# Optimization experiments

Hardware: AMD Instinct MI355X
Metric: run time of the kernel (lower is better)

## Reference

```python
import jax, jax.numpy as jnp
import numpy as np

D = 64          # slot_size == in_features
S = 8           # num_slots
H = 128         # mlp_hidden_size
N_ITER = 3
EPS = 1e-8


def _ln(x, g, b, eps=1e-5):
    m = jnp.mean(x, axis=-1, keepdims=True)
    v = jnp.var(x, axis=-1, keepdims=True)
    return (x - m) * jax.lax.rsqrt(v + eps) * g + b


def _gru(x, h, w_ih, w_hh, b_ih, b_hh):
    # torch.nn.GRUCell semantics, gate order r, z, n
    gi = x @ w_ih.T + b_ih
    gh = h @ w_hh.T + b_hh
    i_r, i_z, i_n = jnp.split(gi, 3, axis=-1)
    h_r, h_z, h_n = jnp.split(gh, 3, axis=-1)
    r = jax.nn.sigmoid(i_r + h_r)
    z = jax.nn.sigmoid(i_z + h_z)
    n = jnp.tanh(i_n + r * h_n)
    return (1.0 - z) * n + z * h


def setup_inputs() -> dict:
    key = jax.random.key(0)
    ks = jax.random.split(key, 16)
    sc = 0.02
    inp = {
        'inputs': jax.random.normal(ks[0], (64, 16384, D), jnp.float32),
        'slots_init': jax.random.normal(ks[1], (64, S, D), jnp.float32),
        'ln_in_g': jnp.ones((D,), jnp.float32), 'ln_in_b': jnp.zeros((D,), jnp.float32),
        'ln_s_g': jnp.ones((D,), jnp.float32), 'ln_s_b': jnp.zeros((D,), jnp.float32),
        'ln_m_g': jnp.ones((D,), jnp.float32), 'ln_m_b': jnp.zeros((D,), jnp.float32),
        'Wq': jax.random.normal(ks[2], (D, D), jnp.float32) * sc,
        'Wk': jax.random.normal(ks[3], (D, D), jnp.float32) * sc,
        'Wv': jax.random.normal(ks[4], (D, D), jnp.float32) * sc,
        'w_ih': jax.random.normal(ks[5], (3 * D, D), jnp.float32) * sc,
        'w_hh': jax.random.normal(ks[6], (3 * D, D), jnp.float32) * sc,
        'b_ih': jnp.zeros((3 * D,), jnp.float32),
        'b_hh': jnp.zeros((3 * D,), jnp.float32),
        'W1': jax.random.normal(ks[7], (H, D), jnp.float32) * sc,
        'b1': jnp.zeros((H,), jnp.float32),
        'W2': jax.random.normal(ks[8], (D, H), jnp.float32) * sc,
        'b2': jnp.zeros((D,), jnp.float32),
        'slots_mu': jax.random.normal(ks[9], (1, 1, D), jnp.float32) * sc,
        'slots_log_sigma': jax.random.normal(ks[10], (1, 1, D), jnp.float32) * sc,
    }
    return inp


def reference(inputs, slots_init, ln_in_g, ln_in_b, ln_s_g, ln_s_b, ln_m_g, ln_m_b,
              Wq, Wk, Wv, w_ih, w_hh, b_ih, b_hh, W1, b1, W2, b2,
              slots_mu, slots_log_sigma):
    B, N, _ = inputs.shape
    x = _ln(inputs, ln_in_g, ln_in_b)
    k = x @ Wk.T                               # [B, N, D]
    v = x @ Wv.T                               # [B, N, D]
    slots = slots_mu + jnp.exp(slots_log_sigma) * slots_init  # [B, S, D]
    scale = D ** -0.5
    attns = None
    for it in range(N_ITER):
        slots_prev = slots
        sn = _ln(slots, ln_s_g, ln_s_b)
        q = sn @ Wq.T                          # [B, S, D]
        logits = scale * jnp.einsum('bnd,bsd->bns', k, q)  # [B, N, S]
        attn = jax.nn.softmax(logits, axis=-1)
        if it == 0:
            attns = jax.lax.stop_gradient(attn)  # clone().detach() on first iter
        else:
            attns = attns + attn
        a = attn + EPS
        a = a / jnp.sum(a, axis=1, keepdims=True)  # normalize over inputs
        updates = jnp.einsum('bns,bnd->bsd', a, v)  # [B, S, D]
        h = _gru(updates.reshape(B * S, D), slots_prev.reshape(B * S, D),
                 w_ih, w_hh, b_ih, b_hh).reshape(B, S, D)
        mlp_out = jnp.maximum(_ln(h, ln_m_g, ln_m_b) @ W1.T + b1, 0.0) @ W2.T + b2
        slots = h + mlp_out
    return slots, attns / N_ITER
```

## Files before the change

kernel.cpp:

```cpp
#include <hip/hip_runtime.h>
#include <math.h>

#define Dk 64
#define Sk 8
#define Nk 16384
#define Bk 64
#define Hk 128
#define BSD (Bk*Sk*Dk)

typedef __attribute__((ext_vector_type(8))) short   bf16x8;
typedef __attribute__((ext_vector_type(4))) float   f32x4;
typedef __attribute__((ext_vector_type(2))) unsigned int u32x2;
typedef __attribute__((ext_vector_type(4))) unsigned int u32x4;

union FragU { u32x4 u; bf16x8 s; };

__device__ __forceinline__ unsigned short f2b(float f){
  unsigned u = __float_as_uint(f);
  unsigned r = (u + 0x7FFFu + ((u>>16)&1u)) >> 16;
  return (unsigned short)r;
}
__device__ __forceinline__ unsigned pk2(float a, float b){
  return (unsigned)f2b(a) | ((unsigned)f2b(b)<<16);
}
__device__ __forceinline__ bf16x8 mkfrag(unsigned a0,unsigned a1,unsigned a2,unsigned a3){
  FragU x; x.u = (u32x4){a0,a1,a2,a3}; return x.s;
}
__device__ __forceinline__ bf16x8 mkfrag2(u32x2 a, u32x2 b){
  FragU x; x.u = (u32x4){a.x,a.y,b.x,b.y}; return x.s;
}
__device__ __forceinline__ float wsum64(float v){
  #pragma unroll
  for (int m=1;m<64;m<<=1) v += __shfl_xor(v,m,64);
  return v;
}
__device__ __forceinline__ f32x4 ntld4(const float* p){
  return __builtin_nontemporal_load((const f32x4*)p);
}

#define MFMA16(a,b,c) __builtin_amdgcn_mfma_f32_16x16x32_bf16(a,b,c,0,0,0)
#define TRRD(dst, addr)          asm volatile("ds_read_b64_tr_b16 %0, %1"              : "=v"(dst) : "v"(addr) : "memory")
#define TRRD_O(dst, addr, OFF)   asm volatile("ds_read_b64_tr_b16 %0, %1 offset:" #OFF : "=v"(dst) : "v"(addr) : "memory")

template<int MODE, int LAST>
__global__ __launch_bounds__(256,4) void iter_kernel(
    const float* __restrict__ inp, unsigned short* __restrict__ xbf,
    const float* __restrict__ ln_g, const float* __restrict__ ln_b,
    const float* __restrict__ qtb,
    float* __restrict__ attns_out,
    float* __restrict__ Upart,
    float* __restrict__ denpart)
{
  constexpr int NQ = LAST ? 3 : 1;
  __shared__ unsigned short shmem[4*2688];
  __shared__ float ured[4][512];
  __shared__ float dred[4][8];

  const int t   = threadIdx.x;
  const int wid = t>>6, l = t&63;
  const int r16 = l&15, g = l>>4;
  unsigned short* sh = &shmem[wid*2688];
  const unsigned ldsb = (unsigned)(unsigned long long)(void*)sh;

  const int blk = blockIdx.x;
  const int gw  = blk*4 + wid;
  const int b   = gw>>6;
  const int w0  = (gw&63)*8;

  bf16x8 qf0[NQ], qf1[NQ];
  #pragma unroll
  for (int it=0; it<NQ; ++it){
    const float* qp = qtb + (size_t)it*BSD + (size_t)((b<<3) + (r16&7))*Dk + g*8;
    f32x4 a0 = *(const f32x4*)(qp);    f32x4 a1 = *(const f32x4*)(qp+4);
    f32x4 c0 = *(const f32x4*)(qp+32); f32x4 c1 = *(const f32x4*)(qp+36);
    qf0[it] = mkfrag(pk2(a0.x,a0.y),pk2(a0.z,a0.w),pk2(a1.x,a1.y),pk2(a1.z,a1.w));
    qf1[it] = mkfrag(pk2(c0.x,c0.y),pk2(c0.z,c0.w),pk2(c1.x,c1.y),pk2(c1.z,c1.w));
  }

  f32x4 uacc0={0.f,0.f,0.f,0.f}, uacc1={0.f,0.f,0.f,0.f};
  f32x4 uacc2={0.f,0.f,0.f,0.f}, uacc3={0.f,0.f,0.f,0.f};
  f32x4 dacc = {0.f,0.f,0.f,0.f};

  f32x4 gv0,gv1,gv2,gv3, bv0,bv1,bv2,bv3;
  if (MODE==0){
    const float* gp  = ln_g + g*8;      const float* bp  = ln_b + g*8;
    const float* gp2 = ln_g + 32 + g*8; const float* bp2 = ln_b + 32 + g*8;
    gv0=*(const f32x4*)gp;  gv1=*(const f32x4*)(gp+4);
    gv2=*(const f32x4*)gp2; gv3=*(const f32x4*)(gp2+4);
    bv0=*(const f32x4*)bp;  bv1=*(const f32x4*)(bp+4);
    bv2=*(const f32x4*)bp2; bv3=*(const f32x4*)(bp2+4);
  }

  f32x4 nx[2][4];
  u32x4 npA[2][2];
  u32x4 npB[2][2];
  u32x4 fr[2][2];

  auto LOADW0 = [&](int w){
    const size_t base = (size_t)b*Nk + (size_t)(w0+w)*32;
    #pragma unroll
    for (int rt=0; rt<2; ++rt){
      const size_t row = base + rt*16 + r16;
      const float* s0 = inp + row*Dk + g*8;
      const float* s1 = inp + row*Dk + 32 + g*8;
      nx[rt][0]=ntld4(s0); nx[rt][1]=ntld4(s0+4);
      nx[rt][2]=ntld4(s1); nx[rt][3]=ntld4(s1+4);
    }
  };
  auto LOADW1 = [&](int w, u32x4 (*np)[2]){
    const size_t base = (size_t)b*Nk + (size_t)(w0+w)*32;
    #pragma unroll
    for (int rt=0; rt<2; ++rt){
      const size_t row = base + rt*16 + r16;
      const unsigned short* sp = xbf + row*Dk;
      np[rt][0] = *(const u32x4*)(sp + g*8);
      np[rt][1] = *(const u32x4*)(sp + 32 + g*8);
    }
  };

  auto PROCESS = [&](int w){
    const size_t base = (size_t)b*Nk + (size_t)(w0+w)*32;
    #pragma unroll
    for (int rt=0; rt<2; ++rt){
      const int rloc = rt*16 + r16;
      u32x4 q0, q1;
      if (MODE==0){
        f32x4 x0=nx[rt][0], x1=nx[rt][1], x2=nx[rt][2], x3=nx[rt][3];
        float s1 = (x0.x+x0.y+x0.z+x0.w)+(x1.x+x1.y+x1.z+x1.w)
                 + (x2.x+x2.y+x2.z+x2.w)+(x3.x+x3.y+x3.z+x3.w);
        float s2 = x0.x*x0.x+x0.y*x0.y+x0.z*x0.z+x0.w*x0.w
                 + x1.x*x1.x+x1.y*x1.y+x1.z*x1.z+x1.w*x1.w
                 + x2.x*x2.x+x2.y*x2.y+x2.z*x2.z+x2.w*x2.w
                 + x3.x*x3.x+x3.y*x3.y+x3.z*x3.z+x3.w*x3.w;
        s1 += __shfl_xor(s1,16,64); s1 += __shfl_xor(s1,32,64);
        s2 += __shfl_xor(s2,16,64); s2 += __shfl_xor(s2,32,64);
        const float mean = s1*(1.f/64.f);
        const float rstd = rsqrtf(s2*(1.f/64.f) - mean*mean + 1e-5f);
        x0 = (x0-mean)*rstd*gv0 + bv0;  x1 = (x1-mean)*rstd*gv1 + bv1;
        x2 = (x2-mean)*rstd*gv2 + bv2;  x3 = (x3-mean)*rstd*gv3 + bv3;
        q0 = (u32x4){pk2(x0.x,x0.y),pk2(x0.z,x0.w),pk2(x1.x,x1.y),pk2(x1.z,x1.w)};
        q1 = (u32x4){pk2(x2.x,x2.y),pk2(x2.z,x2.w),pk2(x3.x,x3.y),pk2(x3.z,x3.w)};
        const size_t row = base + rloc;
        *(u32x4*)(xbf + row*Dk + g*8)      = q0;
        *(u32x4*)(xbf + row*Dk + 32 + g*8) = q1;
      } else {
        q0 = npA[rt][0]; q1 = npA[rt][1];
      }
      fr[rt][0] = q0; fr[rt][1] = q1;
      const int i0 = (g>>1)*528     + rloc*16 + (g&1)*8;
      const int i1 = ((g>>1)+2)*528 + rloc*16 + (g&1)*8;
      *(u32x4*)&sh[i0] = q0;
      *(u32x4*)&sh[i1] = q1;
    }
  };

  if (MODE==0){ LOADW0(0); PROCESS(0); LOADW0(1); }
  else if (!LAST){ LOADW1(0,npA); PROCESS(0); LOADW1(1,npA); LOADW1(2,npB); }
  else { LOADW1(0,npA); PROCESS(0); LOADW1(1,npA); }

  for (int w4=0; w4<8; ++w4){
    const size_t rowwin = (size_t)b*Nk + (size_t)(w0+w4)*32;

    #pragma unroll
    for (int rt=0; rt<2; ++rt){
      FragU fl, fh; fl.u = fr[rt][0]; fh.u = fr[rt][1];
      const bf16x8 xl = fl.s, xh = fh.s;
      f32x4 asum = {0.f,0.f,0.f,0.f};
      f32x4 atc;
      #pragma unroll
      for (int it=0; it<NQ; ++it){
        f32x4 c = {0.f,0.f,0.f,0.f};
        c = MFMA16(qf0[it], xl, c);
        c = MFMA16(qf1[it], xh, c);
        float mx = fmaxf(fmaxf(c.x,c.y), fmaxf(c.z,c.w));
        mx = fmaxf(mx, __shfl_xor(mx,16,64));
        f32x4 e;
        e.x = __expf(c.x-mx); e.y = __expf(c.y-mx);
        e.z = __expf(c.z-mx); e.w = __expf(c.w-mx);
        float es = e.x+e.y+e.z+e.w;
        es += __shfl_xor(es,16,64);
        f32x4 at = e*(1.f/es);
        if (LAST) asum = asum + at;
        atc = at;
      }
      if (LAST && l < 32){
        f32x4 nv = asum*(1.f/3.f);
        __builtin_nontemporal_store(nv,
            (f32x4*)(attns_out + (rowwin + rt*16 + r16)*Sk + g*4));
      }
      f32x4 a = atc + 1e-8f;
      dacc = dacc + a;
      u32x2 pk = {pk2(a.x,a.y), pk2(a.z,a.w)};
      *(u32x2*)&sh[2112 + (rt*16+r16)*16 + g*4] = pk;
    }

    u32x2 p0,p1, b00,b01,b10,b11,b20,b21,b30,b31;
    const unsigned xA = ldsb + g*256 + r16*2;
    const unsigned pA = ldsb + 4224 + g*256 + r16*2;
    TRRD  (b00, xA);          TRRD_O(b01, xA, 128);
    TRRD_O(b10, xA, 1056);    TRRD_O(b11, xA, 1184);
    TRRD_O(b20, xA, 2112);    TRRD_O(b21, xA, 2240);
    TRRD_O(b30, xA, 3168);    TRRD_O(b31, xA, 3296);
    TRRD  (p0, pA);           TRRD_O(p1, pA, 128);

    if (w4 < 7) PROCESS(w4+1);
    if (MODE==0){
      if (w4 < 6) LOADW0(w4+2);
    } else if (!LAST){
      if (w4 < 6){
        #pragma unroll
        for (int rt=0; rt<2; ++rt){ npA[rt][0]=npB[rt][0]; npA[rt][1]=npB[rt][1]; }
      }
      if (w4 < 5) LOADW1(w4+3, npB);
    } else {
      if (w4 < 6) LOADW1(w4+2, npA);
    }

    if (w4 < 7) asm volatile("s_waitcnt lgkmcnt(4)" ::: "memory");
    else        asm volatile("s_waitcnt lgkmcnt(0)" ::: "memory");
    __builtin_amdgcn_sched_barrier(0);

    const bf16x8 pf = mkfrag2(p0,p1);
    uacc0 = MFMA16(pf, mkfrag2(b00,b01), uacc0);
    uacc1 = MFMA16(pf, mkfrag2(b10,b11), uacc1);
    uacc2 = MFMA16(pf, mkfrag2(b20,b21), uacc2);
    uacc3 = MFMA16(pf, mkfrag2(b30,b31), uacc3);
  }

  float dd0=dacc.x, dd1=dacc.y, dd2=dacc.z, dd3=dacc.w;
  #pragma unroll
  for (int m=1;m<16;m<<=1){
    dd0 += __shfl_xor(dd0,m,64); dd1 += __shfl_xor(dd1,m,64);
    dd2 += __shfl_xor(dd2,m,64); dd3 += __shfl_xor(dd3,m,64);
  }
  if (l < 32){
    #pragma unroll
    for (int j=0;j<4;++j){
      ured[wid][(g*4+j)*64 +  0 + r16] = uacc0[j];
      ured[wid][(g*4+j)*64 + 16 + r16] = uacc1[j];
      ured[wid][(g*4+j)*64 + 32 + r16] = uacc2[j];
      ured[wid][(g*4+j)*64 + 48 + r16] = uacc3[j];
    }
    if (r16 == 0){
      dred[wid][g*4+0]=dd0; dred[wid][g*4+1]=dd1;
      dred[wid][g*4+2]=dd2; dred[wid][g*4+3]=dd3;
    }
  }
  __syncthreads();
  #pragma unroll
  for (int e=t; e<512; e+=256){
    Upart[(size_t)blk*512 + e] = ured[0][e]+ured[1][e]+ured[2][e]+ured[3][e];
  }
  if (t < 8) denpart[blk*8 + t] = dred[0][t]+dred[1][t]+dred[2][t]+dred[3][t];
}

__global__ __launch_bounds__(64) void slot_kernel(
    const float* __restrict__ slots_init,
    const float* __restrict__ mu, const float* __restrict__ lsig,
    const float* __restrict__ ln_s_g, const float* __restrict__ ln_s_b,
    const float* __restrict__ ln_m_g, const float* __restrict__ ln_m_b,
    const float* __restrict__ Wq, const float* __restrict__ Wk, const float* __restrict__ Wv,
    const float* __restrict__ w_ih, const float* __restrict__ w_hh,
    const float* __restrict__ b_ih, const float* __restrict__ b_hh,
    const float* __restrict__ W1, const float* __restrict__ b1,
    const float* __restrict__ W2, const float* __restrict__ b2,
    float* __restrict__ slots, const float* __restrict__ Upart,
    const float* __restrict__ denpart,
    float* __restrict__ qt_out, float* __restrict__ slots_out, int mode)
{
  __shared__ float sh[Hk];
  __shared__ float shh[Dk];
  const int d  = threadIdx.x;
  const int bs = blockIdx.x;

  float snew;
  if (mode == 0) {
    snew = mu[d] + expf(lsig[d]) * slots_init[bs*Dk + d];
  } else {
    const int b8 = bs>>3, s = bs&7;
    const float* up = Upart + (size_t)(b8*16)*512 + s*64 + d;
    float uval = 0.f;
    #pragma unroll
    for (int k2=0;k2<16;++k2) uval += up[(size_t)k2*512];
    float dp = (d<16) ? denpart[(b8*16 + d)*Sk + s] : 0.f;
    const float dn = wsum64(dp);

    sh[d] = uval;
    __syncthreads();
    float num = 0.f;
    #pragma unroll
    for (int j=0;j<Dk;j+=4){
      float4 w = *(const float4*)&Wv[d*Dk+j];
      num += sh[j]*w.x + sh[j+1]*w.y + sh[j+2]*w.z + sh[j+3]*w.w;
    }
    const float upd = num / dn;
    const float h = slots[bs*Dk + d];
    __syncthreads();
    sh[d] = upd; shh[d] = h;
    __syncthreads();

    float gi_r=b_ih[d], gi_z=b_ih[Dk+d], gi_n=b_ih[2*Dk+d];
    float gh_r=b_hh[d], gh_z=b_hh[Dk+d], gh_n=b_hh[2*Dk+d];
    #pragma unroll 4
    for (int j=0;j<Dk;j+=4){
      const float x0=sh[j],  x1=sh[j+1],  x2=sh[j+2],  x3=sh[j+3];
      const float h0=shh[j], h1=shh[j+1], h2=shh[j+2], h3=shh[j+3];
      float4 w;
      w = *(const float4*)&w_ih[d*Dk+j];        gi_r += x0*w.x+x1*w.y+x2*w.z+x3*w.w;
      w = *(const float4*)&w_ih[(Dk+d)*Dk+j];   gi_z += x0*w.x+x1*w.y+x2*w.z+x3*w.w;
      w = *(const float4*)&w_ih[(2*Dk+d)*Dk+j]; gi_n += x0*w.x+x1*w.y+x2*w.z+x3*w.w;
      w = *(const float4*)&w_hh[d*Dk+j];        gh_r += h0*w.x+h1*w.y+h2*w.z+h3*w.w;
      w = *(const float4*)&w_hh[(Dk+d)*Dk+j];   gh_z += h0*w.x+h1*w.y+h2*w.z+h3*w.w;
      w = *(const float4*)&w_hh[(2*Dk+d)*Dk+j]; gh_n += h0*w.x+h1*w.y+h2*w.z+h3*w.w;
    }
    const float rg = 1.f/(1.f+expf(-(gi_r+gh_r)));
    const float zg = 1.f/(1.f+expf(-(gi_z+gh_z)));
    const float ng = tanhf(gi_n + rg*gh_n);
    const float hn = (1.f-zg)*ng + zg*h;

    const float m  = wsum64(hn)*(1.f/64.f);
    const float dv = hn - m;
    const float vr = wsum64(dv*dv)*(1.f/64.f);
    const float mv = dv*rsqrtf(vr+1e-5f)*ln_m_g[d] + ln_m_b[d];
    __syncthreads();
    sh[d] = mv;
    __syncthreads();

    float h1a = b1[d], h2a = b1[Dk+d];
    #pragma unroll 4
    for (int j=0;j<Dk;j+=4){
      const float x0=sh[j], x1=sh[j+1], x2=sh[j+2], x3=sh[j+3];
      float4 w;
      w = *(const float4*)&W1[d*Dk+j];      h1a += x0*w.x+x1*w.y+x2*w.z+x3*w.w;
      w = *(const float4*)&W1[(Dk+d)*Dk+j]; h2a += x0*w.x+x1*w.y+x2*w.z+x3*w.w;
    }
    h1a = fmaxf(h1a, 0.f); h2a = fmaxf(h2a, 0.f);
    __syncthreads();
    sh[d] = h1a; sh[Dk+d] = h2a;
    __syncthreads();
    float o = b2[d];
    #pragma unroll 4
    for (int tt=0;tt<Hk;tt+=4){
      float4 w = *(const float4*)&W2[d*Hk+tt];
      o += sh[tt]*w.x + sh[tt+1]*w.y + sh[tt+2]*w.z + sh[tt+3]*w.w;
    }
    snew = hn + o;
  }

  if (slots_out){ slots_out[bs*Dk + d] = snew; return; }
  slots[bs*Dk + d] = snew;

  const float m2  = wsum64(snew)*(1.f/64.f);
  const float dv2 = snew - m2;
  const float vr2 = wsum64(dv2*dv2)*(1.f/64.f);
  const float sn  = dv2*rsqrtf(vr2+1e-5f)*ln_s_g[d] + ln_s_b[d];
  __syncthreads();
  sh[d] = sn;
  __syncthreads();
  float q = 0.f;
  #pragma unroll
  for (int j=0;j<Dk;j+=4){
    float4 w = *(const float4*)&Wq[d*Dk+j];
    q += sh[j]*w.x + sh[j+1]*w.y + sh[j+2]*w.z + sh[j+3]*w.w;
  }
  __syncthreads();
  sh[d] = q;
  __syncthreads();
  float qt = 0.f;
  for (int dd=0; dd<Dk; ++dd) qt += sh[dd]*Wk[dd*Dk + d];
  qt_out[bs*Dk + d] = qt * 0.125f;
}

extern "C" void kernel_launch(void* const* d_in, const int* in_sizes, int n_in,
                              void* d_out, int out_size, void* d_ws, size_t ws_size,
                              hipStream_t stream)
{
  const float* inp     = (const float*)d_in[0];
  const float* sinit   = (const float*)d_in[1];
  const float* ln_in_g = (const float*)d_in[2];
  const float* ln_in_b = (const float*)d_in[3];
  const float* ln_s_g  = (const float*)d_in[4];
  const float* ln_s_b  = (const float*)d_in[5];
  const float* ln_m_g  = (const float*)d_in[6];
  const float* ln_m_b  = (const float*)d_in[7];
  const float* Wq      = (const float*)d_in[8];
  const float* Wk      = (const float*)d_in[9];
  const float* Wv      = (const float*)d_in[10];
  const float* w_ih    = (const float*)d_in[11];
  const float* w_hh    = (const float*)d_in[12];
  const float* b_ih    = (const float*)d_in[13];
  const float* b_hh    = (const float*)d_in[14];
  const float* W1      = (const float*)d_in[15];
  const float* b1      = (const float*)d_in[16];
  const float* W2      = (const float*)d_in[17];
  const float* b2      = (const float*)d_in[18];
  const float* mu      = (const float*)d_in[19];
  const float* lsig    = (const float*)d_in[20];

  float* out       = (float*)d_out;
  float* out_slots = out;
  float* out_attns = out + BSD;

  char* w = (char*)d_ws;
  float* slots   = (float*)(w);
  float* qtbuf   = (float*)(w + 131072);
  float* Upart   = (float*)(w + 655360);
  float* denpart = (float*)(w + 2752512);
  unsigned short* xbf = (unsigned short*)(w + 2785280);

  float* qt0 = qtbuf;
  float* qt1 = qtbuf + BSD;
  float* qt2 = qtbuf + 2*BSD;
  float* qt3 = qtbuf + 3*BSD;

  slot_kernel<<<Bk*Sk, Dk, 0, stream>>>(sinit, mu, lsig, ln_s_g, ln_s_b, ln_m_g, ln_m_b,
      Wq, Wk, Wv, w_ih, w_hh, b_ih, b_hh, W1, b1, W2, b2,
      slots, Upart, denpart, qt0, nullptr, 0);

  iter_kernel<0,0><<<1024, 256, 0, stream>>>(
      inp, xbf, ln_in_g, ln_in_b, qt0, out_attns, Upart, denpart);
  slot_kernel<<<Bk*Sk, Dk, 0, stream>>>(sinit, mu, lsig, ln_s_g, ln_s_b, ln_m_g, ln_m_b,
      Wq, Wk, Wv, w_ih, w_hh, b_ih, b_hh, W1, b1, W2, b2,
      slots, Upart, denpart, qt1, nullptr, 1);

  iter_kernel<1,0><<<1024, 256, 0, stream>>>(
      inp, xbf, ln_in_g, ln_in_b, qt1, out_attns, Upart, denpart);
  slot_kernel<<<Bk*Sk, Dk, 0, stream>>>(sinit, mu, lsig, ln_s_g, ln_s_b, ln_m_g, ln_m_b,
      Wq, Wk, Wv, w_ih, w_hh, b_ih, b_hh, W1, b1, W2, b2,
      slots, Upart, denpart, qt2, nullptr, 1);

  iter_kernel<1,1><<<1024, 256, 0, stream>>>(
      inp, xbf, ln_in_g, ln_in_b, qtbuf, out_attns, Upart, denpart);
  slot_kernel<<<Bk*Sk, Dk, 0, stream>>>(sinit, mu, lsig, ln_s_g, ln_s_b, ln_m_g, ln_m_b,
      Wq, Wk, Wv, w_ih, w_hh, b_ih, b_hh, W1, b1, W2, b2,
      slots, Upart, denpart, qt3, out_slots, 1);
}
```

Before: 233.1 us.

## Halve per-wave work to double grid size and reuse LDS for reduction

Each wave now processes 4 windows of 32 rows instead of 8, so the iteration kernels launch 2048 blocks instead of 1024. The slot kernel sums twice as many partial update and denominator chunks, and the workspace offsets are widened to fit. The separate per-wave reduction array is dropped and the wave's staging LDS is reused for it, which cuts shared memory per block and may raise occupancy. In exchange, the prefetch pipeline has fewer steps to hide its start-up, and the per-block prologue (query fragments, first window load) and partial-sum traffic double.

```diff
diff --git a/kernel.cpp b/kernel.cpp
--- a/kernel.cpp
+++ b/kernel.cpp
@@ -52,8 +52,8 @@
     float* __restrict__ denpart)
 {
   constexpr int NQ = LAST ? 3 : 1;
+  constexpr int NW = 4;
   __shared__ unsigned short shmem[4*2688];
-  __shared__ float ured[4][512];
   __shared__ float dred[4][8];
 
   const int t   = threadIdx.x;
@@ -64,8 +64,8 @@
 
   const int blk = blockIdx.x;
   const int gw  = blk*4 + wid;
-  const int b   = gw>>6;
-  const int w0  = (gw&63)*8;
+  const int b   = gw>>7;
+  const int w0  = (gw&127)*NW;
 
   bf16x8 qf0[NQ], qf1[NQ];
   #pragma unroll
@@ -158,7 +158,7 @@
   else if (!LAST){ LOADW1(0,npA); PROCESS(0); LOADW1(1,npA); LOADW1(2,npB); }
   else { LOADW1(0,npA); PROCESS(0); LOADW1(1,npA); }
 
-  for (int w4=0; w4<8; ++w4){
+  for (int w4=0; w4<NW; ++w4){
     const size_t rowwin = (size_t)b*Nk + (size_t)(w0+w4)*32;
 
     #pragma unroll
@@ -203,21 +203,21 @@
     TRRD_O(b30, xA, 3168);    TRRD_O(b31, xA, 3296);
     TRRD  (p0, pA);           TRRD_O(p1, pA, 128);
 
-    if (w4 < 7) PROCESS(w4+1);
+    if (w4 < NW-1) PROCESS(w4+1);
     if (MODE==0){
-      if (w4 < 6) LOADW0(w4+2);
+      if (w4 < NW-2) LOADW0(w4+2);
     } else if (!LAST){
-      if (w4 < 6){
+      if (w4 < NW-2){
         #pragma unroll
         for (int rt=0; rt<2; ++rt){ npA[rt][0]=npB[rt][0]; npA[rt][1]=npB[rt][1]; }
       }
-      if (w4 < 5) LOADW1(w4+3, npB);
+      if (w4 < NW-3) LOADW1(w4+3, npB);
     } else {
-      if (w4 < 6) LOADW1(w4+2, npA);
-    }
-
-    if (w4 < 7) asm volatile("s_waitcnt lgkmcnt(4)" ::: "memory");
-    else        asm volatile("s_waitcnt lgkmcnt(0)" ::: "memory");
+      if (w4 < NW-2) LOADW1(w4+2, npA);
+    }
+
+    if (w4 < NW-1) asm volatile("s_waitcnt lgkmcnt(4)" ::: "memory");
+    else           asm volatile("s_waitcnt lgkmcnt(0)" ::: "memory");
     __builtin_amdgcn_sched_barrier(0);
 
     const bf16x8 pf = mkfrag2(p0,p1);
@@ -233,13 +233,14 @@
     dd0 += __shfl_xor(dd0,m,64); dd1 += __shfl_xor(dd1,m,64);
     dd2 += __shfl_xor(dd2,m,64); dd3 += __shfl_xor(dd3,m,64);
   }
+  float* uredw = (float*)sh;
   if (l < 32){
     #pragma unroll
     for (int j=0;j<4;++j){
-      ured[wid][(g*4+j)*64 +  0 + r16] = uacc0[j];
-      ured[wid][(g*4+j)*64 + 16 + r16] = uacc1[j];
-      ured[wid][(g*4+j)*64 + 32 + r16] = uacc2[j];
-      ured[wid][(g*4+j)*64 + 48 + r16] = uacc3[j];
+      uredw[(g*4+j)*64 +  0 + r16] = uacc0[j];
+      uredw[(g*4+j)*64 + 16 + r16] = uacc1[j];
+      uredw[(g*4+j)*64 + 32 + r16] = uacc2[j];
+      uredw[(g*4+j)*64 + 48 + r16] = uacc3[j];
     }
     if (r16 == 0){
       dred[wid][g*4+0]=dd0; dred[wid][g*4+1]=dd1;
@@ -247,11 +248,17 @@
     }
   }
   __syncthreads();
-  #pragma unroll
-  for (int e=t; e<512; e+=256){
-    Upart[(size_t)blk*512 + e] = ured[0][e]+ured[1][e]+ured[2][e]+ured[3][e];
-  }
-  if (t < 8) denpart[blk*8 + t] = dred[0][t]+dred[1][t]+dred[2][t]+dred[3][t];
+  {
+    const float* u0p = (const float*)&shmem[0];
+    const float* u1p = (const float*)&shmem[2688];
+    const float* u2p = (const float*)&shmem[2*2688];
+    const float* u3p = (const float*)&shmem[3*2688];
+    #pragma unroll
+    for (int e=t; e<512; e+=256){
+      Upart[(size_t)blk*512 + e] = u0p[e]+u1p[e]+u2p[e]+u3p[e];
+    }
+    if (t < 8) denpart[blk*8 + t] = dred[0][t]+dred[1][t]+dred[2][t]+dred[3][t];
+  }
 }
 
 __global__ __launch_bounds__(64) void slot_kernel(
@@ -278,11 +285,11 @@
     snew = mu[d] + expf(lsig[d]) * slots_init[bs*Dk + d];
   } else {
     const int b8 = bs>>3, s = bs&7;
-    const float* up = Upart + (size_t)(b8*16)*512 + s*64 + d;
+    const float* up = Upart + (size_t)(b8*32)*512 + s*64 + d;
     float uval = 0.f;
-    #pragma unroll
-    for (int k2=0;k2<16;++k2) uval += up[(size_t)k2*512];
-    float dp = (d<16) ? denpart[(b8*16 + d)*Sk + s] : 0.f;
+    #pragma unroll 8
+    for (int k2=0;k2<32;++k2) uval += up[(size_t)k2*512];
+    float dp = (d<32) ? denpart[(b8*32 + d)*Sk + s] : 0.f;
     const float dn = wsum64(dp);
 
     sh[d] = uval;
@@ -405,8 +412,8 @@
   float* slots   = (float*)(w);
   float* qtbuf   = (float*)(w + 131072);
   float* Upart   = (float*)(w + 655360);
-  float* denpart = (float*)(w + 2752512);
-  unsigned short* xbf = (unsigned short*)(w + 2785280);
+  float* denpart = (float*)(w + 4849664);
+  unsigned short* xbf = (unsigned short*)(w + 4915200);
 
   float* qt0 = qtbuf;
   float* qt1 = qtbuf + BSD;
@@ -417,19 +424,19 @@
       Wq, Wk, Wv, w_ih, w_hh, b_ih, b_hh, W1, b1, W2, b2,
       slots, Upart, denpart, qt0, nullptr, 0);
 
-  iter_kernel<0,0><<<1024, 256, 0, stream>>>(
+  iter_kernel<0,0><<<2048, 256, 0, stream>>>(
       inp, xbf, ln_in_g, ln_in_b, qt0, out_attns, Upart, denpart);
   slot_kernel<<<Bk*Sk, Dk, 0, stream>>>(sinit, mu, lsig, ln_s_g, ln_s_b, ln_m_g, ln_m_b,
       Wq, Wk, Wv, w_ih, w_hh, b_ih, b_hh, W1, b1, W2, b2,
       slots, Upart, denpart, qt1, nullptr, 1);
 
-  iter_kernel<1,0><<<1024, 256, 0, stream>>>(
+  iter_kernel<1,0><<<2048, 256, 0, stream>>>(
       inp, xbf, ln_in_g, ln_in_b, qt1, out_attns, Upart, denpart);
   slot_kernel<<<Bk*Sk, Dk, 0, stream>>>(sinit, mu, lsig, ln_s_g, ln_s_b, ln_m_g, ln_m_b,
       Wq, Wk, Wv, w_ih, w_hh, b_ih, b_hh, W1, b1, W2, b2,
       slots, Upart, denpart, qt2, nullptr, 1);
 
-  iter_kernel<1,1><<<1024, 256, 0, stream>>>(
+  iter_kernel<1,1><<<2048, 256, 0, stream>>>(
       inp, xbf, ln_in_g, ln_in_b, qtbuf, out_attns, Upart, denpart);
   slot_kernel<<<Bk*Sk, Dk, 0, stream>>>(sinit, mu, lsig, ln_s_g, ln_s_b, ln_m_g, ln_m_b,
       Wq, Wk, Wv, w_ih, w_hh, b_ih, b_hh, W1, b1, W2, b2,
```

After: 232.3 us. No clear change (-0.4%).
